# Performance work log

Hardware: AMD Instinct MI355X
Metric: run time of the kernel (lower is better)

## Reference

```python
import jax, jax.numpy as jnp
import numpy as np

N_CELLS, D_IN, D_HID, D_OUT, MLP_W = 16384, 512, 1024, 512, 128
N_FACTIONS, SYNC, DEBATE = 8, 0.15, 0.15


def setup_inputs() -> dict:
    key = jax.random.key(0)
    ks = jax.random.split(key, 20)
    s = 0.05
    inp = {
        "x": jax.random.normal(ks[0], (1, D_IN), jnp.float32),
        "hiddens": jax.random.normal(ks[1], (N_CELLS, D_HID), jnp.float32) * 0.1,
        "wealth_norm": jax.random.uniform(ks[2], (N_CELLS,), jnp.float32, 0.5, 1.5),
        "Wa1": jax.random.normal(ks[3], (D_IN + D_HID, MLP_W), jnp.float32) * s,
        "ba1": jax.random.normal(ks[4], (MLP_W,), jnp.float32) * s,
        "Wa2": jax.random.normal(ks[5], (MLP_W, D_OUT), jnp.float32) * s,
        "ba2": jax.random.normal(ks[6], (D_OUT,), jnp.float32) * s,
        "Wg1": jax.random.normal(ks[7], (D_IN + D_HID, MLP_W), jnp.float32) * s,
        "bg1": jax.random.normal(ks[8], (MLP_W,), jnp.float32) * s,
        "Wg2": jax.random.normal(ks[9], (MLP_W, D_OUT), jnp.float32) * s,
        "bg2": jax.random.normal(ks[10], (D_OUT,), jnp.float32) * s,
        "W_ih": jax.random.normal(ks[11], (D_OUT + 1, 3 * D_HID), jnp.float32) * s,
        "W_hh": jax.random.normal(ks[12], (D_HID, 3 * D_HID), jnp.float32) * s,
        "b_ih": jax.random.normal(ks[13], (3 * D_HID,), jnp.float32) * s,
        "b_hh": jax.random.normal(ks[14], (3 * D_HID,), jnp.float32) * s,
        "Wo": jax.random.normal(ks[15], (D_OUT, D_IN), jnp.float32) * s,
        "bo": jax.random.normal(ks[16], (D_IN,), jnp.float32) * s,
        "positions": jax.random.randint(ks[17], (N_CELLS,), 0, 3, jnp.int32) - 1,
        "step": 10,
    }
    return inp


def _gru_cell(mem, h, W_ih, W_hh, b_ih, b_hh):
    # torch.nn.GRUCell math, gate order r, z, n
    gi = mem @ W_ih + b_ih            # [N, 3H]
    gh = h @ W_hh + b_hh              # [N, 3H]
    gi_r, gi_z, gi_n = jnp.split(gi, 3, axis=-1)
    gh_r, gh_z, gh_n = jnp.split(gh, 3, axis=-1)
    r = jax.nn.sigmoid(gi_r + gh_r)
    z = jax.nn.sigmoid(gi_z + gh_z)
    n = jnp.tanh(gi_n + r * gh_n)
    return (1.0 - z) * n + z * h


def _group_sync(h, mask):
    cnt = jnp.sum(mask)
    m = mask[:, None].astype(h.dtype)
    mean = jnp.sum(h * m, axis=0) / jnp.maximum(cnt, 1).astype(h.dtype)
    blended = 0.9 * h + 0.1 * mean
    return jnp.where((mask[:, None]) & (cnt >= 2), blended, h)


def _faction_sync_debate(h, step):
    n = h.shape[0]
    n_f = min(N_FACTIONS, n // 2)
    if n_f < 2:
        return h
    fs = n // n_f
    hf = h[: n_f * fs].reshape(n_f, fs, -1)
    fmean = hf.mean(axis=1, keepdims=True)                    # [n_f, 1, H]
    hf = (1.0 - SYNC) * hf + SYNC * fmean
    if step > 5:
        global_op = hf.mean(axis=1).mean(axis=0)              # [H]
        dc = max(1, fs // 4)
        head = (1.0 - DEBATE) * hf[:, :dc] + DEBATE * global_op
        hf = jnp.concatenate([head, hf[:, dc:]], axis=1)
    out = hf.reshape(n_f * fs, -1)
    if n_f * fs < n:
        out = jnp.concatenate([out, h[n_f * fs:]], axis=0)
    return out


def reference(x, hiddens, wealth_norm, Wa1, ba1, Wa2, ba2, Wg1, bg1, Wg2, bg2,
              W_ih, W_hh, b_ih, b_hh, Wo, bo, positions, step):
    n = hiddens.shape[0]
    xb = jnp.broadcast_to(x, (n, x.shape[-1]))                # same x for every cell
    combined = jnp.concatenate([xb, hiddens], axis=-1)        # [N, D_in+D_hid]
    a = jax.nn.relu(combined @ Wa1 + ba1) @ Wa2 + ba2
    g = jax.nn.relu(combined @ Wg1 + bg1) @ Wg2 + bg2
    output = a - g                                            # [N, D_out]
    tension = jnp.mean(output ** 2, axis=-1, keepdims=True)   # [N, 1]
    mem_input = jax.lax.stop_gradient(jnp.concatenate([output, tension], axis=-1))
    new_h = _gru_cell(mem_input, hiddens, W_ih, W_hh, b_ih, b_hh)
    mod = 0.9 + 0.1 * jnp.clip(wealth_norm, 0.1, 2.0)
    new_h = jnp.clip(new_h * mod[:, None], -10.0, 10.0)
    new_h = jax.lax.stop_gradient(new_h)                      # original detaches state
    new_h = _group_sync(new_h, positions > 0)
    new_h = _group_sync(new_h, positions < 0)
    new_h = _faction_sync_debate(new_h, step)
    # tension weights come from .item() in torch -> constants
    weights = jax.nn.softmax(jax.lax.stop_gradient(tension[:, 0]))
    combined_out = weights @ output                           # [D_out]
    pred = (combined_out @ Wo + bo)[None, :]                  # [1, D_in]
    avg_tension = jnp.mean(tension)
    return pred, avg_tension, new_h
```

## Files before the change

kernel.cpp:

```cpp
#include <hip/hip_runtime.h>
#include <stdint.h>

typedef unsigned short u16;
typedef __bf16 bf16x8 __attribute__((ext_vector_type(8)));
typedef float f32x4 __attribute__((ext_vector_type(4)));


__device__ __forceinline__ float bf2f(unsigned u) { return __uint_as_float(u << 16); }
__device__ __forceinline__ u16 f2bf(float f) {
  unsigned x = __float_as_uint(f);
  unsigned r = x + 0x7fffu + ((x >> 16) & 1u);
  return (u16)(r >> 16);
}
__device__ __forceinline__ float sigm(float x) { return 1.f / (1.f + __expf(-x)); }
__device__ __forceinline__ float fast_tanh(float x) {
  float e = __expf(2.f * x);
  return 1.f - 2.f / (e + 1.f);
}

#define AS1(p) ((const __attribute__((address_space(1))) void*)(p))
#define AS3(p) ((__attribute__((address_space(3))) void*)(p))

#define NC 16384

__device__ __forceinline__ void packT_body(
    const float* __restrict__ src, int sld, int srow0,
    u16* __restrict__ dst, int dld, int drow0, int koff,
    int remapThresh, int remapAdd, float sgn, int bx, int by,
    float (*tile)[65], int t) {
  const int k0 = by * 64, c0 = bx * 64;
  const int tx = t & 15, ty = t >> 4;
#pragma unroll
  for (int p = 0; p < 4; ++p) {
    int r = ty + p * 16;
    float4 v = *reinterpret_cast<const float4*>(&src[(size_t)(srow0 + k0 + r) * sld + c0 + tx * 4]);
    tile[tx * 4 + 0][r] = v.x;
    tile[tx * 4 + 1][r] = v.y;
    tile[tx * 4 + 2][r] = v.z;
    tile[tx * 4 + 3][r] = v.w;
  }
  __syncthreads();
  const int cl = t >> 2;
  const int kb = (t & 3) * 16;
  int col = c0 + cl;
  int row = drow0 + col + ((col >= remapThresh) ? remapAdd : 0);
  union { u16 o[16]; uint4 v[2]; } u;
#pragma unroll
  for (int e = 0; e < 16; ++e) u.o[e] = f2bf(sgn * tile[cl][kb + e]);
  uint4* d = reinterpret_cast<uint4*>(&dst[(size_t)row * dld + koff + k0 + kb]);
  d[0] = u.v[0]; d[1] = u.v[1];
}

__global__ __launch_bounds__(256) void prep_kernel(
    const float* __restrict__ hid, u16* __restrict__ hidc,
    const float* __restrict__ W_ih, const float* __restrict__ W_hh, u16* __restrict__ WgruT,
    const float* __restrict__ Wa1, const float* __restrict__ Wg1, u16* __restrict__ W1catT,
    const float* __restrict__ Wa2, const float* __restrict__ Wg2, u16* __restrict__ W2catT) {
  __shared__ float tile[64][65];
  int b = blockIdx.x, t = threadIdx.x;
  if (b < 8192) {
    int i = b * 256 + t;
    const float4* s = (const float4*)hid;
    float4 a = s[(size_t)i * 2], c = s[(size_t)i * 2 + 1];
    union { u16 o[8]; uint4 v; } u;
    u.o[0] = f2bf(a.x); u.o[1] = f2bf(a.y); u.o[2] = f2bf(a.z); u.o[3] = f2bf(a.w);
    u.o[4] = f2bf(c.x); u.o[5] = f2bf(c.y); u.o[6] = f2bf(c.z); u.o[7] = f2bf(c.w);
    ((uint4*)hidc)[i] = u.v;
    return;
  }
  b -= 8192;
  if (b < 768) {
    packT_body(W_hh, 3072, 0, WgruT, 1536, 0, 512, 2048, 1024, 1.f, b % 48, b / 48, tile, t);
    return;
  }
  b -= 768;
  if (b < 384) {
    packT_body(W_ih, 3072, 0, WgruT, 1536, 0, 0, 1 << 30, 0, 1.f, b % 48, b / 48, tile, t);
    return;
  }
  b -= 384;
  if (b < 32) {
    packT_body(Wa1, 128, 512, W1catT, 1024, 0, 0, 1 << 30, 0, 1.f, b % 2, b / 2, tile, t);
    return;
  }
  b -= 32;
  if (b < 32) {
    packT_body(Wg1, 128, 512, W1catT, 1024, 128, 0, 1 << 30, 0, 1.f, b % 2, b / 2, tile, t);
    return;
  }
  b -= 32;
  if (b < 16) {
    packT_body(Wa2, 512, 0, W2catT, 256, 0, 0, 1 << 30, 0, 1.f, b % 8, b / 8, tile, t);
    return;
  }
  b -= 16;
  packT_body(Wg2, 512, 0, W2catT, 256, 0, 128, 1 << 30, 0, -1.f, b % 8, b / 8, tile, t);
}

__global__ void smalls_kernel(const float* __restrict__ x, const float* __restrict__ Wa1,
                              const float* __restrict__ ba1, const float* __restrict__ Wg1,
                              const float* __restrict__ bg1, float* __restrict__ bias1,
                              const float* __restrict__ ba2, const float* __restrict__ bg2,
                              float* __restrict__ bias2, const int* __restrict__ positions,
                              int* __restrict__ counts) {
  int b = blockIdx.x, t = threadIdx.x;
  if (b < 8) {
    const float* W = (t < 128) ? Wa1 : Wg1;
    int cc = t & 127;
    float acc = 0.f;
    int k0 = b * 64;
    for (int k = k0; k < k0 + 64; ++k) acc += x[k] * W[(size_t)k * 128 + cc];
    if (b == 0) acc += (t < 128) ? ba1[cc] : bg1[cc];
    atomicAdd(&bias1[t], acc);
  } else if (b < 10) {
    int n = (b - 8) * 256 + t;
    bias2[n] = ba2[n] - bg2[n];
  } else {
    int i = (b - 10) * 256 + t;
    int p = positions[i], f = i >> 11;
    if (p > 0) atomicAdd(&counts[f * 2], 1);
    else if (p < 0) atomicAdd(&counts[f * 2 + 1], 1);
  }
}

__global__ __launch_bounds__(256) void gemm_bt(
    const u16* __restrict__ A, int lda,
    const u16* __restrict__ Bt, int ldb,
    u16* __restrict__ C, int ldc,
    const float* __restrict__ bias, int epi, int K,
    float* __restrict__ tension) {
  __shared__ __align__(16) u16 As[128 * 32];
  __shared__ __align__(16) u16 Bs[128 * 32];
  const int tid = threadIdx.x;
  const int m0 = blockIdx.x * 128;
  const int n0 = blockIdx.y * 128;
  f32x4 acc[4][4] = {};
  const int lane = tid & 63;
  const int w = tid >> 6;
  const int mw = (w & 1) * 64, nw = (w >> 1) * 64;
  const int fr = lane & 15;
  const int kq = (lane >> 4) * 8;
  const int ar0 = tid >> 2, ak0 = (tid & 3) * 8;
  const int ar1 = ar0 + 64;

  for (int kk = 0; kk < K; kk += 32) {
    __syncthreads();
    __builtin_amdgcn_global_load_lds(AS1(A + (size_t)(m0 + ar0) * lda + kk + ak0), AS3(&As[tid * 8]), 16, 0, 0);
    __builtin_amdgcn_global_load_lds(AS1(A + (size_t)(m0 + ar1) * lda + kk + ak0), AS3(&As[(tid + 256) * 8]), 16, 0, 0);
    __builtin_amdgcn_global_load_lds(AS1(Bt + (size_t)(n0 + ar0) * ldb + kk + ak0), AS3(&Bs[tid * 8]), 16, 0, 0);
    __builtin_amdgcn_global_load_lds(AS1(Bt + (size_t)(n0 + ar1) * ldb + kk + ak0), AS3(&Bs[(tid + 256) * 8]), 16, 0, 0);
    __syncthreads();
    bf16x8 af[4], bfv[4];
#pragma unroll
    for (int mt = 0; mt < 4; ++mt)
      af[mt] = *reinterpret_cast<const bf16x8*>(&As[(mw + mt * 16 + fr) * 32 + kq]);
#pragma unroll
    for (int nt = 0; nt < 4; ++nt)
      bfv[nt] = *reinterpret_cast<const bf16x8*>(&Bs[(nw + nt * 16 + fr) * 32 + kq]);
#pragma unroll
    for (int mt = 0; mt < 4; ++mt)
#pragma unroll
      for (int nt = 0; nt < 4; ++nt)
        acc[mt][nt] = __builtin_amdgcn_mfma_f32_16x16x32_bf16(af[mt], bfv[nt], acc[mt][nt], 0, 0, 0);
  }
  const int rq = (lane >> 4) * 4;
#pragma unroll
  for (int mt = 0; mt < 4; ++mt) {
    float srow[4] = {0.f, 0.f, 0.f, 0.f};
#pragma unroll
    for (int nt = 0; nt < 4; ++nt) {
      int col = n0 + nw + nt * 16 + fr;
      f32x4 v = acc[mt][nt];
#pragma unroll
      for (int r = 0; r < 4; ++r) {
        int row = m0 + mw + mt * 16 + rq + r;
        float val = v[r] + bias[col];
        if (epi == 1) val = val > 0.f ? val : 0.f;
        else srow[r] += val * val;
        C[(size_t)row * ldc + col] = f2bf(val);
      }
    }
    if (epi == 3) {
#pragma unroll
      for (int r = 0; r < 4; ++r) {
        float s = srow[r];
        s += __shfl_xor(s, 1, 16); s += __shfl_xor(s, 2, 16);
        s += __shfl_xor(s, 4, 16); s += __shfl_xor(s, 8, 16);
        if (fr == 0) atomicAdd(&tension[m0 + mw + mt * 16 + rq + r], s);
      }
    }
  }
}

__global__ __launch_bounds__(256, 2) void gemm_gru(
    const u16* __restrict__ outbf, const u16* __restrict__ hidc,
    const u16* __restrict__ WgruT,
    const float* __restrict__ W_ihf, const float* __restrict__ bihf,
    const float* __restrict__ bhhf, const float* __restrict__ wealthf,
    const float* __restrict__ tension, u16* __restrict__ hpre) {
  __shared__ __align__(16) u16 As[128 * 32];
  __shared__ __align__(16) u16 Bs[3][64 * 32];
  const int tid = threadIdx.x;
  const int m0 = blockIdx.x * 128;
  const int j0 = blockIdx.y * 64;
  f32x4 acc[4][4][2] = {};
  const int lane = tid & 63;
  const int w = tid >> 6;
  const int mw = (w & 1) * 64, nw = (w >> 1) * 32;
  const int fr = lane & 15;
  const int kq = (lane >> 4) * 8;
  const int ar0 = tid >> 2, ak0 = (tid & 3) * 8;
  const int ar1 = ar0 + 64;

  auto kstep = [&](const u16* Ap, int lda, int ka, int growBase, int gi) {
    __syncthreads();
    __builtin_amdgcn_global_load_lds(AS1(Ap + (size_t)(m0 + ar0) * lda + ka + ak0), AS3(&As[tid * 8]), 16, 0, 0);
    __builtin_amdgcn_global_load_lds(AS1(Ap + (size_t)(m0 + ar1) * lda + ka + ak0), AS3(&As[(tid + 256) * 8]), 16, 0, 0);
    (void)growBase; (void)gi;
  };
  (void)kstep;

#pragma unroll 1
  for (int phase = 0; phase < 2; ++phase) {
    const u16* Ap = phase ? hidc : outbf;
    const int lda = phase ? 1024 : 512;
    const int kbeg = phase ? 512 : 0;
    const int kend = phase ? 1536 : 512;
    const int growG = phase ? 3072 : 2048;
#pragma unroll 1
    for (int kk = kbeg; kk < kend; kk += 32) {
      __syncthreads();
      int ka = kk - kbeg;
      __builtin_amdgcn_global_load_lds(AS1(Ap + (size_t)(m0 + ar0) * lda + ka + ak0), AS3(&As[tid * 8]), 16, 0, 0);
      __builtin_amdgcn_global_load_lds(AS1(Ap + (size_t)(m0 + ar1) * lda + ka + ak0), AS3(&As[(tid + 256) * 8]), 16, 0, 0);
      __builtin_amdgcn_global_load_lds(AS1(WgruT + (size_t)(j0 + ar0) * 1536 + kk + ak0), AS3(&Bs[0][tid * 8]), 16, 0, 0);
      __builtin_amdgcn_global_load_lds(AS1(WgruT + (size_t)(1024 + j0 + ar0) * 1536 + kk + ak0), AS3(&Bs[1][tid * 8]), 16, 0, 0);
      __builtin_amdgcn_global_load_lds(AS1(WgruT + (size_t)(growG + j0 + ar0) * 1536 + kk + ak0), AS3(&Bs[2][tid * 8]), 16, 0, 0);
      __syncthreads();
      bf16x8 af[4], b0[2], b1[2], b2[2];
#pragma unroll
      for (int mt = 0; mt < 4; ++mt)
        af[mt] = *reinterpret_cast<const bf16x8*>(&As[(mw + mt * 16 + fr) * 32 + kq]);
#pragma unroll
      for (int nt = 0; nt < 2; ++nt) {
        b0[nt] = *reinterpret_cast<const bf16x8*>(&Bs[0][(nw + nt * 16 + fr) * 32 + kq]);
        b1[nt] = *reinterpret_cast<const bf16x8*>(&Bs[1][(nw + nt * 16 + fr) * 32 + kq]);
        b2[nt] = *reinterpret_cast<const bf16x8*>(&Bs[2][(nw + nt * 16 + fr) * 32 + kq]);
      }
      int greg = phase ? 3 : 2;
#pragma unroll
      for (int mt = 0; mt < 4; ++mt)
#pragma unroll
        for (int nt = 0; nt < 2; ++nt) {
          acc[0][mt][nt] = __builtin_amdgcn_mfma_f32_16x16x32_bf16(af[mt], b0[nt], acc[0][mt][nt], 0, 0, 0);
          acc[1][mt][nt] = __builtin_amdgcn_mfma_f32_16x16x32_bf16(af[mt], b1[nt], acc[1][mt][nt], 0, 0, 0);
          acc[greg][mt][nt] = __builtin_amdgcn_mfma_f32_16x16x32_bf16(af[mt], b2[nt], acc[greg][mt][nt], 0, 0, 0);
        }
    }
  }

  const int rq = (lane >> 4) * 4;
  const float* wt = W_ihf + (size_t)512 * 3072;
  float wtr[2], wtz[2], wtn[2], bir[2], biz[2], bin_[2], bhr_[2], bhz_[2], bhn_[2];
#pragma unroll
  for (int nt = 0; nt < 2; ++nt) {
    int j = j0 + nw + nt * 16 + fr;
    wtr[nt] = wt[j]; wtz[nt] = wt[1024 + j]; wtn[nt] = wt[2048 + j];
    bir[nt] = bihf[j]; biz[nt] = bihf[1024 + j]; bin_[nt] = bihf[2048 + j];
    bhr_[nt] = bhhf[j]; bhz_[nt] = bhhf[1024 + j]; bhn_[nt] = bhhf[2048 + j];
  }
#pragma unroll
  for (int mt = 0; mt < 4; ++mt) {
#pragma unroll
    for (int rr = 0; rr < 4; ++rr) {
      int row = m0 + mw + mt * 16 + rq + rr;
      float tv = tension[row] * (1.f / 512.f);
      float wl = fminf(fmaxf(wealthf[row], 0.1f), 2.0f);
      float mod = 0.9f + 0.1f * wl;
#pragma unroll
      for (int nt = 0; nt < 2; ++nt) {
        int j = j0 + nw + nt * 16 + fr;
        float r = sigm(acc[0][mt][nt][rr] + tv * wtr[nt] + bir[nt] + bhr_[nt]);
        float z = sigm(acc[1][mt][nt][rr] + tv * wtz[nt] + biz[nt] + bhz_[nt]);
        float n = fast_tanh(acc[2][mt][nt][rr] + tv * wtn[nt] + bin_[nt]
                            + r * (acc[3][mt][nt][rr] + bhn_[nt]));
        float h = bf2f(hidc[(size_t)row * 1024 + j]);
        float h2 = (1.f - z) * n + z * h;
        h2 = fminf(fmaxf(h2 * mod, -10.f), 10.f);
        hpre[(size_t)row * 1024 + j] = f2bf(h2);
      }
    }
  }
}

__global__ void stats_kernel(const u16* __restrict__ hpre, const int* __restrict__ positions,
                             float* __restrict__ fsums) {
  int cc = blockIdx.x, f = blockIdx.y, z = blockIdx.z, t = threadIdx.x;
  int col = cc * 128 + (t & 127);
  int half = t >> 7;
  float st = 0, sp = 0, sm = 0;
  for (int it = 0; it < 128; ++it) {
    int row = (f << 11) + ((z * 128 + it) << 1) + half;
    int p = positions[row];
    float v = bf2f(hpre[(size_t)row * 1024 + col]);
    st += v;
    if (p > 0) sp += v;
    if (p < 0) sm += v;
  }
  atomicAdd(&fsums[(f * 3 + 0) * 1024 + col], st);
  atomicAdd(&fsums[(f * 3 + 1) * 1024 + col], sp);
  atomicAdd(&fsums[(f * 3 + 2) * 1024 + col], sm);
}

__global__ void derive_kernel(const float* __restrict__ fsums, const int* __restrict__ counts,
                              float* __restrict__ mean1, float* __restrict__ mean2,
                              float* __restrict__ fmean, float* __restrict__ gop,
                              float* __restrict__ scal) {
  int c = threadIdx.x;
  int cnt1 = 0, cnt2 = 0, cf1[8], cf2[8];
#pragma unroll
  for (int f = 0; f < 8; ++f) {
    cf1[f] = counts[f * 2]; cf2[f] = counts[f * 2 + 1];
    cnt1 += cf1[f]; cnt2 += cf2[f];
  }
  float s1 = 0, s2 = 0;
#pragma unroll
  for (int f = 0; f < 8; ++f) { s1 += fsums[(f * 3 + 1) * 1024 + c]; s2 += fsums[(f * 3 + 2) * 1024 + c]; }
  float m1 = s1 / (float)(cnt1 > 1 ? cnt1 : 1);
  float m2 = s2 / (float)(cnt2 > 1 ? cnt2 : 1);
  float a1 = (cnt1 >= 2) ? 0.1f : 0.f;
  float a2 = (cnt2 >= 2) ? 0.1f : 0.f;
  float g = 0;
#pragma unroll
  for (int f = 0; f < 8; ++f) {
    float fm = (fsums[(f * 3) * 1024 + c]
                + a1 * ((float)cf1[f] * m1 - fsums[(f * 3 + 1) * 1024 + c])
                + a2 * ((float)cf2[f] * m2 - fsums[(f * 3 + 2) * 1024 + c])) * (1.f / 2048.f);
    fmean[f * 1024 + c] = fm;
    g += fm;
  }
  gop[c] = g * 0.125f;
  mean1[c] = m1; mean2[c] = m2;
  if (c == 0) { scal[0] = a1; scal[1] = a2; }
}

__global__ void finalize_kernel(const u16* __restrict__ hpre, const int* __restrict__ positions,
                                const int* __restrict__ step, const float* __restrict__ mean1,
                                const float* __restrict__ mean2, const float* __restrict__ fmean,
                                const float* __restrict__ gop, const float* __restrict__ scal,
                                float* __restrict__ out) {
  int row = blockIdx.x, t = threadIdx.x;
  int p = positions[row];
  float w1 = (p > 0) ? scal[0] : 0.f;
  float w2 = (p < 0) ? scal[1] : 0.f;
  int f = row >> 11, q = row & 2047;
  bool deb = (step[0] > 5) && (q < 512);
  const u16* hrow = hpre + (size_t)row * 1024;
  const float* fmp = fmean + f * 1024;
  float* orow = out + 513 + (size_t)row * 1024;
#pragma unroll
  for (int e = 0; e < 8; ++e) {
    int c = e * 128 + t;
    float h = bf2f(hrow[c]);
    float hgs = h + w1 * (mean1[c] - h) + w2 * (mean2[c] - h);
    float hfs = 0.85f * hgs + 0.15f * fmp[c];
    orow[c] = deb ? (0.85f * hfs + 0.15f * gop[c]) : hfs;
  }
}

__global__ void softmax_kernel(const float* __restrict__ tension, float* __restrict__ weights,
                               float* __restrict__ out) {
  __shared__ float red[1024];
  int t = threadIdx.x;
  float tv[16], mx = -1e30f, sumt = 0.f;
#pragma unroll
  for (int k = 0; k < 16; ++k) {
    tv[k] = tension[t + k * 1024] * (1.f / 512.f);
    mx = fmaxf(mx, tv[k]); sumt += tv[k];
  }
  red[t] = mx; __syncthreads();
  for (int s = 512; s > 0; s >>= 1) { if (t < s) red[t] = fmaxf(red[t], red[t + s]); __syncthreads(); }
  float m = red[0]; __syncthreads();
  red[t] = sumt; __syncthreads();
  for (int s = 512; s > 0; s >>= 1) { if (t < s) red[t] += red[t + s]; __syncthreads(); }
  float tot = red[0]; __syncthreads();
  float ev[16], se = 0.f;
#pragma unroll
  for (int k = 0; k < 16; ++k) { ev[k] = __expf(tv[k] - m); se += ev[k]; }
  red[t] = se; __syncthreads();
  for (int s = 512; s > 0; s >>= 1) { if (t < s) red[t] += red[t + s]; __syncthreads(); }
  float invS = 1.f / red[0];
#pragma unroll
  for (int k = 0; k < 16; ++k) weights[t + k * 1024] = ev[k] * invS;
  if (t == 0) out[512] = tot * (1.f / 16384.f);
}

__global__ void wsum_kernel(const float* __restrict__ weights, const u16* __restrict__ outbf,
                            float* __restrict__ co) {
  int b = blockIdx.x, t = threadIdx.x;
  int c = t * 2;
  float a0 = 0.f, a1 = 0.f;
  int i0 = b * 128;
  for (int i = i0; i < i0 + 128; ++i) {
    float w = weights[i];
    unsigned v = *reinterpret_cast<const unsigned*>(outbf + (size_t)i * 512 + c);
    a0 += w * bf2f(v & 0xffff);
    a1 += w * bf2f(v >> 16);
  }
  atomicAdd(&co[c], a0);
  atomicAdd(&co[c + 1], a1);
}

__global__ void pred_kernel(const float* __restrict__ co, const float* __restrict__ Wof,
                            const float* __restrict__ bof, float* __restrict__ out) {
  __shared__ float cs[512];
  int t = threadIdx.x, n = blockIdx.x * 256 + t;
  cs[t] = co[t]; cs[t + 256] = co[t + 256];
  __syncthreads();
  float acc = bof[n];
  for (int ck = 0; ck < 512; ++ck) acc += cs[ck] * Wof[(size_t)ck * 512 + n];
  out[n] = acc;
}

extern "C" void kernel_launch(void* const* d_in, const int* in_sizes, int n_in,
                              void* d_out, int out_size, void* d_ws, size_t ws_size,
                              hipStream_t stream) {
  const float* x      = (const float*)d_in[0];
  const float* hid    = (const float*)d_in[1];
  const float* wealth = (const float*)d_in[2];
  const float* Wa1    = (const float*)d_in[3];
  const float* ba1    = (const float*)d_in[4];
  const float* Wa2    = (const float*)d_in[5];
  const float* ba2    = (const float*)d_in[6];
  const float* Wg1    = (const float*)d_in[7];
  const float* bg1    = (const float*)d_in[8];
  const float* Wg2    = (const float*)d_in[9];
  const float* bg2    = (const float*)d_in[10];
  const float* W_ih   = (const float*)d_in[11];
  const float* W_hh   = (const float*)d_in[12];
  const float* b_ih   = (const float*)d_in[13];
  const float* b_hh   = (const float*)d_in[14];
  const float* Wo     = (const float*)d_in[15];
  const float* bo     = (const float*)d_in[16];
  const int* positions= (const int*)d_in[17];
  const int* step     = (const int*)d_in[18];
  float* out = (float*)d_out;

  char* w = (char*)d_ws;
  size_t off = 0;
  auto alloc = [&](size_t bytes) { void* p = w + off; off += (bytes + 255) & ~(size_t)255; return p; };
  u16*   hidc    = (u16*)  alloc((size_t)NC * 1024 * 2);
  u16*   outbf   = (u16*)  alloc((size_t)NC * 512 * 2);
  u16*   hpre    = (u16*)  alloc((size_t)NC * 1024 * 2);
  u16*   WgruT   = (u16*)  alloc((size_t)4096 * 1536 * 2);
  u16*   W1catT  = (u16*)  alloc((size_t)256 * 1024 * 2);
  u16*   W2catT  = (u16*)  alloc((size_t)512 * 256 * 2);
  u16*   t1      = (u16*)  alloc((size_t)NC * 256 * 2);
  float* bias1   = (float*)alloc(256 * 4);
  float* co      = (float*)alloc(512 * 4);
  int*   counts  = (int*)  alloc(16 * 4);
  float* fsums   = (float*)alloc(8 * 3 * 1024 * 4);
  float* tension = (float*)alloc(NC * 4);
  float* bias2   = (float*)alloc(512 * 4);
  float* weights = (float*)alloc(NC * 4);
  float* mean1   = (float*)alloc(1024 * 4);
  float* mean2   = (float*)alloc(1024 * 4);
  float* gop     = (float*)alloc(1024 * 4);
  float* fmean   = (float*)alloc(8 * 1024 * 4);
  float* scal    = (float*)alloc(8 * 4);

  hipMemsetAsync(bias1, 0, 1024 + 2048 + 256 + 98304 + 65536, stream);

  prep_kernel<<<9440, 256, 0, stream>>>(hid, hidc, W_ih, W_hh, WgruT,
                                        Wa1, Wg1, W1catT, Wa2, Wg2, W2catT);
  smalls_kernel<<<74, 256, 0, stream>>>(x, Wa1, ba1, Wg1, bg1, bias1,
                                        ba2, bg2, bias2, positions, counts);

  gemm_bt<<<dim3(128, 2), 256, 0, stream>>>(hidc, 1024, W1catT, 1024, t1, 256,
                                            bias1, 1, 1024, nullptr);
  gemm_bt<<<dim3(128, 4), 256, 0, stream>>>(t1, 256, W2catT, 256, outbf, 512,
                                            bias2, 3, 256, tension);

  gemm_gru<<<dim3(128, 16), 256, 0, stream>>>(outbf, hidc, WgruT, W_ih, b_ih, b_hh,
                                              wealth, tension, hpre);

  stats_kernel<<<dim3(8, 8, 8), 256, 0, stream>>>(hpre, positions, fsums);
  derive_kernel<<<1, 1024, 0, stream>>>(fsums, counts, mean1, mean2, fmean, gop, scal);
  finalize_kernel<<<NC, 128, 0, stream>>>(hpre, positions, step, mean1, mean2, fmean, gop,
                                          scal, out);

  softmax_kernel<<<1, 1024, 0, stream>>>(tension, weights, out);
  wsum_kernel<<<128, 256, 0, stream>>>(weights, outbf, co);
  pred_kernel<<<2, 256, 0, stream>>>(co, Wo, bo, out);

  (void)in_sizes; (void)n_in; (void)out_size; (void)ws_size;
}
```

Before: 630.1 us.

## Swizzle LDS tiles, widen GRU GEMM to 512 threads, merge small kernels into prep

An XOR swizzle is applied to the LDS layout of the A/B tiles in both GEMMs to reduce bank conflicts on the fragment reads. The GRU GEMM moves to 512 threads per block with 8 waves, each holding a 32x32 sub-tile, and the weight-gate loads are split between the two thread halves. This lowers per-thread register pressure and aims for higher occupancy. The smalls kernel is folded into the prep kernel to save a launch, and hidden-state conversion now uses narrower per-thread work over twice as many blocks.

```diff
diff --git a/kernel.cpp b/kernel.cpp
--- a/kernel.cpp
+++ b/kernel.cpp
@@ -11,6 +11,9 @@
   unsigned x = __float_as_uint(f);
   unsigned r = x + 0x7fffu + ((x >> 16) & 1u);
   return (u16)(r >> 16);
+}
+__device__ __forceinline__ unsigned pack2(float a, float b) {
+  return (unsigned)f2bf(a) | ((unsigned)f2bf(b) << 16);
 }
 __device__ __forceinline__ float sigm(float x) { return 1.f / (1.f + __expf(-x)); }
 __device__ __forceinline__ float fast_tanh(float x) {
@@ -55,20 +58,20 @@
     const float* __restrict__ hid, u16* __restrict__ hidc,
     const float* __restrict__ W_ih, const float* __restrict__ W_hh, u16* __restrict__ WgruT,
     const float* __restrict__ Wa1, const float* __restrict__ Wg1, u16* __restrict__ W1catT,
-    const float* __restrict__ Wa2, const float* __restrict__ Wg2, u16* __restrict__ W2catT) {
+    const float* __restrict__ Wa2, const float* __restrict__ Wg2, u16* __restrict__ W2catT,
+    const float* __restrict__ x, const float* __restrict__ ba1, const float* __restrict__ bg1,
+    float* __restrict__ bias1, const float* __restrict__ ba2, const float* __restrict__ bg2,
+    float* __restrict__ bias2, const int* __restrict__ positions, int* __restrict__ counts) {
   __shared__ float tile[64][65];
   int b = blockIdx.x, t = threadIdx.x;
-  if (b < 8192) {
+  if (b < 16384) {
     int i = b * 256 + t;
-    const float4* s = (const float4*)hid;
-    float4 a = s[(size_t)i * 2], c = s[(size_t)i * 2 + 1];
-    union { u16 o[8]; uint4 v; } u;
-    u.o[0] = f2bf(a.x); u.o[1] = f2bf(a.y); u.o[2] = f2bf(a.z); u.o[3] = f2bf(a.w);
-    u.o[4] = f2bf(c.x); u.o[5] = f2bf(c.y); u.o[6] = f2bf(c.z); u.o[7] = f2bf(c.w);
-    ((uint4*)hidc)[i] = u.v;
+    float4 v = ((const float4*)hid)[i];
+    uint2 o; o.x = pack2(v.x, v.y); o.y = pack2(v.z, v.w);
+    ((uint2*)hidc)[i] = o;
     return;
   }
-  b -= 8192;
+  b -= 16384;
   if (b < 768) {
     packT_body(W_hh, 3072, 0, WgruT, 1536, 0, 512, 2048, 1024, 1.f, b % 48, b / 48, tile, t);
     return;
@@ -79,31 +82,14 @@
     return;
   }
   b -= 384;
-  if (b < 32) {
-    packT_body(Wa1, 128, 512, W1catT, 1024, 0, 0, 1 << 30, 0, 1.f, b % 2, b / 2, tile, t);
-    return;
-  }
+  if (b < 32) { packT_body(Wa1, 128, 512, W1catT, 1024, 0, 0, 1 << 30, 0, 1.f, b % 2, b / 2, tile, t); return; }
   b -= 32;
-  if (b < 32) {
-    packT_body(Wg1, 128, 512, W1catT, 1024, 128, 0, 1 << 30, 0, 1.f, b % 2, b / 2, tile, t);
-    return;
-  }
+  if (b < 32) { packT_body(Wg1, 128, 512, W1catT, 1024, 128, 0, 1 << 30, 0, 1.f, b % 2, b / 2, tile, t); return; }
   b -= 32;
-  if (b < 16) {
-    packT_body(Wa2, 512, 0, W2catT, 256, 0, 0, 1 << 30, 0, 1.f, b % 8, b / 8, tile, t);
-    return;
-  }
+  if (b < 16) { packT_body(Wa2, 512, 0, W2catT, 256, 0, 0, 1 << 30, 0, 1.f, b % 8, b / 8, tile, t); return; }
   b -= 16;
-  packT_body(Wg2, 512, 0, W2catT, 256, 0, 128, 1 << 30, 0, -1.f, b % 8, b / 8, tile, t);
-}
-
-__global__ void smalls_kernel(const float* __restrict__ x, const float* __restrict__ Wa1,
-                              const float* __restrict__ ba1, const float* __restrict__ Wg1,
-                              const float* __restrict__ bg1, float* __restrict__ bias1,
-                              const float* __restrict__ ba2, const float* __restrict__ bg2,
-                              float* __restrict__ bias2, const int* __restrict__ positions,
-                              int* __restrict__ counts) {
-  int b = blockIdx.x, t = threadIdx.x;
+  if (b < 16) { packT_body(Wg2, 512, 0, W2catT, 256, 0, 128, 1 << 30, 0, -1.f, b % 8, b / 8, tile, t); return; }
+  b -= 16;
   if (b < 8) {
     const float* W = (t < 128) ? Wa1 : Wg1;
     int cc = t & 127;
@@ -112,11 +98,13 @@
     for (int k = k0; k < k0 + 64; ++k) acc += x[k] * W[(size_t)k * 128 + cc];
     if (b == 0) acc += (t < 128) ? ba1[cc] : bg1[cc];
     atomicAdd(&bias1[t], acc);
-  } else if (b < 10) {
-    int n = (b - 8) * 256 + t;
-    bias2[n] = ba2[n] - bg2[n];
-  } else {
-    int i = (b - 10) * 256 + t;
+    return;
+  }
+  b -= 8;
+  if (b < 2) { int n = b * 256 + t; bias2[n] = ba2[n] - bg2[n]; return; }
+  b -= 2;
+  {
+    int i = b * 256 + t;
     int p = positions[i], f = i >> 11;
     if (p > 0) atomicAdd(&counts[f * 2], 1);
     else if (p < 0) atomicAdd(&counts[f * 2 + 1], 1);
@@ -139,31 +127,35 @@
   const int w = tid >> 6;
   const int mw = (w & 1) * 64, nw = (w >> 1) * 64;
   const int fr = lane & 15;
-  const int kq = (lane >> 4) * 8;
-  const int ar0 = tid >> 2, ak0 = (tid & 3) * 8;
-  const int ar1 = ar0 + 64;
+  const int q = lane >> 4;
+  const int ar0 = tid >> 2;
+  const int ag = ((tid & 3) ^ ((ar0 >> 1) & 3)) * 8;
 
   for (int kk = 0; kk < K; kk += 32) {
     __syncthreads();
-    __builtin_amdgcn_global_load_lds(AS1(A + (size_t)(m0 + ar0) * lda + kk + ak0), AS3(&As[tid * 8]), 16, 0, 0);
-    __builtin_amdgcn_global_load_lds(AS1(A + (size_t)(m0 + ar1) * lda + kk + ak0), AS3(&As[(tid + 256) * 8]), 16, 0, 0);
-    __builtin_amdgcn_global_load_lds(AS1(Bt + (size_t)(n0 + ar0) * ldb + kk + ak0), AS3(&Bs[tid * 8]), 16, 0, 0);
-    __builtin_amdgcn_global_load_lds(AS1(Bt + (size_t)(n0 + ar1) * ldb + kk + ak0), AS3(&Bs[(tid + 256) * 8]), 16, 0, 0);
+    __builtin_amdgcn_global_load_lds(AS1(A + (size_t)(m0 + ar0) * lda + kk + ag), AS3(&As[tid * 8]), 16, 0, 0);
+    __builtin_amdgcn_global_load_lds(AS1(A + (size_t)(m0 + ar0 + 64) * lda + kk + ag), AS3(&As[(tid + 256) * 8]), 16, 0, 0);
+    __builtin_amdgcn_global_load_lds(AS1(Bt + (size_t)(n0 + ar0) * ldb + kk + ag), AS3(&Bs[tid * 8]), 16, 0, 0);
+    __builtin_amdgcn_global_load_lds(AS1(Bt + (size_t)(n0 + ar0 + 64) * ldb + kk + ag), AS3(&Bs[(tid + 256) * 8]), 16, 0, 0);
     __syncthreads();
     bf16x8 af[4], bfv[4];
 #pragma unroll
-    for (int mt = 0; mt < 4; ++mt)
-      af[mt] = *reinterpret_cast<const bf16x8*>(&As[(mw + mt * 16 + fr) * 32 + kq]);
-#pragma unroll
-    for (int nt = 0; nt < 4; ++nt)
-      bfv[nt] = *reinterpret_cast<const bf16x8*>(&Bs[(nw + nt * 16 + fr) * 32 + kq]);
+    for (int mt = 0; mt < 4; ++mt) {
+      int r = mw + mt * 16 + fr;
+      af[mt] = *reinterpret_cast<const bf16x8*>(&As[r * 32 + ((q ^ ((r >> 1) & 3)) * 8)]);
+    }
+#pragma unroll
+    for (int nt = 0; nt < 4; ++nt) {
+      int r = nw + nt * 16 + fr;
+      bfv[nt] = *reinterpret_cast<const bf16x8*>(&Bs[r * 32 + ((q ^ ((r >> 1) & 3)) * 8)]);
+    }
 #pragma unroll
     for (int mt = 0; mt < 4; ++mt)
 #pragma unroll
       for (int nt = 0; nt < 4; ++nt)
         acc[mt][nt] = __builtin_amdgcn_mfma_f32_16x16x32_bf16(af[mt], bfv[nt], acc[mt][nt], 0, 0, 0);
   }
-  const int rq = (lane >> 4) * 4;
+  const int rq = q * 4;
 #pragma unroll
   for (int mt = 0; mt < 4; ++mt) {
     float srow[4] = {0.f, 0.f, 0.f, 0.f};
@@ -192,7 +184,7 @@
   }
 }
 
-__global__ __launch_bounds__(256, 2) void gemm_gru(
+__global__ __launch_bounds__(512, 4) void gemm_gru(
     const u16* __restrict__ outbf, const u16* __restrict__ hidc,
     const u16* __restrict__ WgruT,
     const float* __restrict__ W_ihf, const float* __restrict__ bihf,
@@ -203,24 +195,20 @@
   const int tid = threadIdx.x;
   const int m0 = blockIdx.x * 128;
   const int j0 = blockIdx.y * 64;
-  f32x4 acc[4][4][2] = {};
+  f32x4 acc[4][2][2] = {};
   const int lane = tid & 63;
   const int w = tid >> 6;
-  const int mw = (w & 1) * 64, nw = (w >> 1) * 32;
+  const int mw = (w & 3) * 32, nw = (w >> 2) * 32;
   const int fr = lane & 15;
-  const int kq = (lane >> 4) * 8;
-  const int ar0 = tid >> 2, ak0 = (tid & 3) * 8;
-  const int ar1 = ar0 + 64;
-
-  auto kstep = [&](const u16* Ap, int lda, int ka, int growBase, int gi) {
-    __syncthreads();
-    __builtin_amdgcn_global_load_lds(AS1(Ap + (size_t)(m0 + ar0) * lda + ka + ak0), AS3(&As[tid * 8]), 16, 0, 0);
-    __builtin_amdgcn_global_load_lds(AS1(Ap + (size_t)(m0 + ar1) * lda + ka + ak0), AS3(&As[(tid + 256) * 8]), 16, 0, 0);
-    (void)growBase; (void)gi;
-  };
-  (void)kstep;
-
-#pragma unroll 1
+  const int q = lane >> 4;
+  const int arow = tid >> 2;
+  const int ag = ((tid & 3) ^ ((arow >> 1) & 3)) * 8;
+  const int ct = tid & 255;
+  const int brow = ct >> 2;
+  const int bg = ((ct & 3) ^ ((brow >> 1) & 3)) * 8;
+  const int bsel = tid >> 8;
+
+#pragma unroll
   for (int phase = 0; phase < 2; ++phase) {
     const u16* Ap = phase ? hidc : outbf;
     const int lda = phase ? 1024 : 512;
@@ -229,37 +217,45 @@
     const int growG = phase ? 3072 : 2048;
 #pragma unroll 1
     for (int kk = kbeg; kk < kend; kk += 32) {
+      const int ka = kk - kbeg;
       __syncthreads();
-      int ka = kk - kbeg;
-      __builtin_amdgcn_global_load_lds(AS1(Ap + (size_t)(m0 + ar0) * lda + ka + ak0), AS3(&As[tid * 8]), 16, 0, 0);
-      __builtin_amdgcn_global_load_lds(AS1(Ap + (size_t)(m0 + ar1) * lda + ka + ak0), AS3(&As[(tid + 256) * 8]), 16, 0, 0);
-      __builtin_amdgcn_global_load_lds(AS1(WgruT + (size_t)(j0 + ar0) * 1536 + kk + ak0), AS3(&Bs[0][tid * 8]), 16, 0, 0);
-      __builtin_amdgcn_global_load_lds(AS1(WgruT + (size_t)(1024 + j0 + ar0) * 1536 + kk + ak0), AS3(&Bs[1][tid * 8]), 16, 0, 0);
-      __builtin_amdgcn_global_load_lds(AS1(WgruT + (size_t)(growG + j0 + ar0) * 1536 + kk + ak0), AS3(&Bs[2][tid * 8]), 16, 0, 0);
+      __builtin_amdgcn_global_load_lds(AS1(Ap + (size_t)(m0 + arow) * lda + ka + ag), AS3(&As[tid * 8]), 16, 0, 0);
+      if (bsel == 0) {
+        __builtin_amdgcn_global_load_lds(AS1(WgruT + (size_t)(j0 + brow) * 1536 + kk + bg), AS3(&Bs[0][ct * 8]), 16, 0, 0);
+        __builtin_amdgcn_global_load_lds(AS1(WgruT + (size_t)(growG + j0 + brow) * 1536 + kk + bg), AS3(&Bs[2][ct * 8]), 16, 0, 0);
+      } else {
+        __builtin_amdgcn_global_load_lds(AS1(WgruT + (size_t)(1024 + j0 + brow) * 1536 + kk + bg), AS3(&Bs[1][ct * 8]), 16, 0, 0);
+      }
       __syncthreads();
-      bf16x8 af[4], b0[2], b1[2], b2[2];
-#pragma unroll
-      for (int mt = 0; mt < 4; ++mt)
-        af[mt] = *reinterpret_cast<const bf16x8*>(&As[(mw + mt * 16 + fr) * 32 + kq]);
+      bf16x8 af[2], b0[2], b1[2], b2[2];
+#pragma unroll
+      for (int mt = 0; mt < 2; ++mt) {
+        int r = mw + mt * 16 + fr;
+        af[mt] = *reinterpret_cast<const bf16x8*>(&As[r * 32 + ((q ^ ((r >> 1) & 3)) * 8)]);
+      }
 #pragma unroll
       for (int nt = 0; nt < 2; ++nt) {
-        b0[nt] = *reinterpret_cast<const bf16x8*>(&Bs[0][(nw + nt * 16 + fr) * 32 + kq]);
-        b1[nt] = *reinterpret_cast<const bf16x8*>(&Bs[1][(nw + nt * 16 + fr) * 32 + kq]);
-        b2[nt] = *reinterpret_cast<const bf16x8*>(&Bs[2][(nw + nt * 16 + fr) * 32 + kq]);
-      }
-      int greg = phase ? 3 : 2;
-#pragma unroll
-      for (int mt = 0; mt < 4; ++mt)
+        int r = nw + nt * 16 + fr;
+        int s = (q ^ ((r >> 1) & 3)) * 8;
+        b0[nt] = *reinterpret_cast<const bf16x8*>(&Bs[0][r * 32 + s]);
+        b1[nt] = *reinterpret_cast<const bf16x8*>(&Bs[1][r * 32 + s]);
+        b2[nt] = *reinterpret_cast<const bf16x8*>(&Bs[2][r * 32 + s]);
+      }
+#pragma unroll
+      for (int mt = 0; mt < 2; ++mt)
 #pragma unroll
         for (int nt = 0; nt < 2; ++nt) {
           acc[0][mt][nt] = __builtin_amdgcn_mfma_f32_16x16x32_bf16(af[mt], b0[nt], acc[0][mt][nt], 0, 0, 0);
           acc[1][mt][nt] = __builtin_amdgcn_mfma_f32_16x16x32_bf16(af[mt], b1[nt], acc[1][mt][nt], 0, 0, 0);
-          acc[greg][mt][nt] = __builtin_amdgcn_mfma_f32_16x16x32_bf16(af[mt], b2[nt], acc[greg][mt][nt], 0, 0, 0);
+          if (phase == 0)
+            acc[2][mt][nt] = __builtin_amdgcn_mfma_f32_16x16x32_bf16(af[mt], b2[nt], acc[2][mt][nt], 0, 0, 0);
+          else
+            acc[3][mt][nt] = __builtin_amdgcn_mfma_f32_16x16x32_bf16(af[mt], b2[nt], acc[3][mt][nt], 0, 0, 0);
         }
     }
   }
 
-  const int rq = (lane >> 4) * 4;
+  const int rq = q * 4;
   const float* wt = W_ihf + (size_t)512 * 3072;
   float wtr[2], wtz[2], wtn[2], bir[2], biz[2], bin_[2], bhr_[2], bhz_[2], bhn_[2];
 #pragma unroll
@@ -270,7 +266,7 @@
     bhr_[nt] = bhhf[j]; bhz_[nt] = bhhf[1024 + j]; bhn_[nt] = bhhf[2048 + j];
   }
 #pragma unroll
-  for (int mt = 0; mt < 4; ++mt) {
+  for (int mt = 0; mt < 2; ++mt) {
 #pragma unroll
     for (int rr = 0; rr < 4; ++rr) {
       int row = m0 + mw + mt * 16 + rq + rr;
@@ -471,17 +467,17 @@
 
   hipMemsetAsync(bias1, 0, 1024 + 2048 + 256 + 98304 + 65536, stream);
 
-  prep_kernel<<<9440, 256, 0, stream>>>(hid, hidc, W_ih, W_hh, WgruT,
-                                        Wa1, Wg1, W1catT, Wa2, Wg2, W2catT);
-  smalls_kernel<<<74, 256, 0, stream>>>(x, Wa1, ba1, Wg1, bg1, bias1,
-                                        ba2, bg2, bias2, positions, counts);
+  prep_kernel<<<17706, 256, 0, stream>>>(hid, hidc, W_ih, W_hh, WgruT,
+                                         Wa1, Wg1, W1catT, Wa2, Wg2, W2catT,
+                                         x, ba1, bg1, bias1, ba2, bg2, bias2,
+                                         positions, counts);
 
   gemm_bt<<<dim3(128, 2), 256, 0, stream>>>(hidc, 1024, W1catT, 1024, t1, 256,
                                             bias1, 1, 1024, nullptr);
   gemm_bt<<<dim3(128, 4), 256, 0, stream>>>(t1, 256, W2catT, 256, outbf, 512,
                                             bias2, 3, 256, tension);
 
-  gemm_gru<<<dim3(128, 16), 256, 0, stream>>>(outbf, hidc, WgruT, W_ih, b_ih, b_hh,
+  gemm_gru<<<dim3(128, 16), 512, 0, stream>>>(outbf, hidc, WgruT, W_ih, b_ih, b_hh,
                                               wealth, tension, hpre);
 
   stats_kernel<<<dim3(8, 8, 8), 256, 0, stream>>>(hpre, positions, fsums);
```

After: 604.4 us. -4.1%, faster.
